# Performance work log

Hardware: AMD Instinct MI355X
Metric: run time of the kernel (lower is better)

## Reference

```python
import jax, jax.numpy as jnp
import numpy as np

N_G, N_D, D = 50000, 50000, 64
R, L, NNZ, B = 32, 2, 1600000, 2048
TEMP, LAMBDA_1, LAMBDA_2, DROPOUT = 0.2, 0.2, 1e-7, 0.1


def setup_inputs() -> dict:
    key = jax.random.key(0)
    ks = jax.random.split(key, 14)
    uids = jax.random.randint(ks[0], (B,), 0, N_G)
    iids = jax.random.randint(ks[1], (B,), 0, N_D)
    pos = jax.random.randint(ks[2], (B,), 0, N_D)
    neg = jax.random.randint(ks[3], (B,), 0, N_D)
    E_g_0 = jax.random.normal(ks[4], (N_G, D), jnp.float32) * 0.01
    E_d_0 = jax.random.normal(ks[5], (N_D, D), jnp.float32) * 0.01
    rows = jax.random.randint(ks[6], (NNZ,), 0, N_G)
    cols = jax.random.randint(ks[7], (NNZ,), 0, N_D)
    vals = jax.random.uniform(ks[8], (NNZ,), jnp.float32)
    g_mul_s = jax.random.normal(ks[9], (N_G, R), jnp.float32) * 0.1
    v_mul_s = jax.random.normal(ks[10], (N_D, R), jnp.float32) * 0.1
    ut = jax.random.normal(ks[11], (R, N_G), jnp.float32) * (N_G ** -0.5)
    vt = jax.random.normal(ks[12], (R, N_D), jnp.float32) * (N_D ** -0.5)
    drop_u = jax.random.uniform(ks[13], (L, 2, NNZ), jnp.float32)
    return {"uids": uids, "iids": iids, "pos": pos, "neg": neg,
            "E_g_0": E_g_0, "E_d_0": E_d_0, "rows": rows, "cols": cols,
            "vals": vals, "g_mul_s": g_mul_s, "v_mul_s": v_mul_s,
            "ut": ut, "vt": vt, "drop_u": drop_u}


def reference(uids, iids, pos, neg, E_g_0, E_d_0, rows, cols, vals,
              g_mul_s, v_mul_s, ut, vt, drop_u):
    # sparse_dropout keep masks (independent per layer and per spmm call)
    keep = (drop_u > DROPOUT).astype(vals.dtype) / (1.0 - DROPOUT)  # [L,2,NNZ]
    E_g, E_d = E_g_0, E_d_0
    E_g_sum, E_d_sum = E_g_0, E_d_0
    G_g_sum, G_d_sum = E_g_0, E_d_0
    for layer in range(L):
        # Z_g = dropout(A) @ E_d ; Z_d = dropout(A).T @ E_g  (COO spmm)
        vg = vals * keep[layer, 0]
        Z_g = jax.ops.segment_sum(vg[:, None] * E_d[cols], rows, num_segments=N_G)
        vd = vals * keep[layer, 1]
        Z_d = jax.ops.segment_sum(vd[:, None] * E_g[rows], cols, num_segments=N_D)
        # low-rank SVD branch
        G_g = g_mul_s @ (vt @ E_d)  # [n_g, d]
        G_d = v_mul_s @ (ut @ E_g)  # [n_d, d]
        E_g, E_d = Z_g, Z_d
        E_g_sum = E_g_sum + E_g
        E_d_sum = E_d_sum + E_d
        G_g_sum = G_g_sum + G_g
        G_d_sum = G_d_sum + G_d
    # InfoNCE-style contrastive loss (exactly as torch: log(sum exp + eps))
    S_g = (G_g_sum[uids] @ E_g_sum.T) / TEMP  # [B, n_g]
    S_d = (G_d_sum[iids] @ E_d_sum.T) / TEMP  # [B, n_d]
    neg_score = jnp.log(jnp.exp(S_g).sum(1) + 1e-8).mean() \
              + jnp.log(jnp.exp(S_d).sum(1) + 1e-8).mean()
    pos_score = jnp.clip((G_g_sum[uids] * E_g_sum[uids]).sum(1) / TEMP, -5.0, 5.0).mean() \
              + jnp.clip((G_d_sum[iids] * E_d_sum[iids]).sum(1) / TEMP, -5.0, 5.0).mean()
    loss_s = -pos_score + neg_score
    # BPR loss
    g_emb = E_g_sum[uids]
    diff = (g_emb * E_d_sum[pos]).sum(-1) - (g_emb * E_d_sum[neg]).sum(-1)
    loss_r = -jnp.log(jax.nn.sigmoid(diff)).mean()
    # L2 reg over trainable embedding params
    loss_reg = LAMBDA_2 * (jnp.sum(E_g_0 ** 2) + jnp.sum(E_d_0 ** 2))
    loss = loss_r + LAMBDA_1 * loss_s + loss_reg
    return (loss, loss_r, LAMBDA_1 * loss_s)
```

## Files before the change

kernel.cpp:

```cpp
#include <hip/hip_runtime.h>
#include <hip/hip_bf16.h>
#include <math.h>

#define N_Gc 50000
#define N_Dc 50000
#define DIM 64
#define RNK 32
#define NNZc 1600000
#define BSZ 2048
#define KEEPV (1.0f/0.9f)
#define INVT 5.0f
#define NBK3 391
#define NBLK 200
#define NSL 48
#define EPB 8000
#define MCH 256
#define MBLK 196
#define SCAP 6144

typedef __attribute__((ext_vector_type(8))) short bfrag;
typedef __attribute__((ext_vector_type(4))) float f32x4;
typedef unsigned long long u64;

__device__ inline ushort f2bf(float f) {
  union { float f; unsigned int u; } v; v.f = f;
  unsigned int r = (v.u + 0x7fffu + ((v.u >> 16) & 1u)) >> 16;
  return (ushort)r;
}
__device__ inline float bf2f(ushort u) {
  union { unsigned int i; float f; } v; v.i = ((unsigned int)u) << 16;
  return v.f;
}

__global__ __launch_bounds__(256) void hist3_kernel(const int* __restrict__ rows, const int* __restrict__ cols,
                                                    int* __restrict__ cntR, int* __restrict__ cntC) {
  __shared__ int lh_r[NBK3];
  __shared__ int lh_c[NBK3];
  int t = threadIdx.x, blk = blockIdx.x;
  for (int j = t; j < NBK3; j += 256) { lh_r[j] = 0; lh_c[j] = 0; }
  __syncthreads();
  int e0 = blk*EPB;
  for (int i = e0 + t; i < e0 + EPB; i += 256) {
    atomicAdd(&lh_r[__builtin_nontemporal_load(&rows[i]) >> 7], 1);
    atomicAdd(&lh_c[__builtin_nontemporal_load(&cols[i]) >> 7], 1);
  }
  __syncthreads();
  for (int j = t; j < NBK3; j += 256) {
    cntR[j*NBLK + blk] = lh_r[j];
    cntC[j*NBLK + blk] = lh_c[j];
  }
}

__global__ __launch_bounds__(1024) void cscan2_kernel(const int* __restrict__ cntA, int* __restrict__ cbA, int* __restrict__ bpA,
                                                      const int* __restrict__ cntB, int* __restrict__ cbB, int* __restrict__ bpB) {
  const int n = NBK3*NBLK;
  const int* cnt = blockIdx.x ? cntB : cntA;
  int* cb = blockIdx.x ? cbB : cbA;
  int* bp = blockIdx.x ? bpB : bpA;
  __shared__ int wsum[16];
  int t = threadIdx.x, lane = t & 63, w = t >> 6;
  int carry = 0;
  for (int base = 0; base < n; base += 1024) {
    int i = base + t;
    int v = (i < n) ? cnt[i] : 0;
    int x = v;
    #pragma unroll
    for (int o = 1; o < 64; o <<= 1) { int y = __shfl_up(x, o); if (lane >= o) x += y; }
    if (lane == 63) wsum[w] = x;
    __syncthreads();
    if (t < 16) {
      int s = wsum[t];
      #pragma unroll
      for (int o = 1; o < 16; o <<= 1) { int y = __shfl_up(s, o); if (t >= o) s += y; }
      wsum[t] = s;
    }
    __syncthreads();
    int wpre = (w == 0) ? 0 : wsum[w-1];
    int total = wsum[15];
    int ex = carry + wpre + (x - v);
    if (i < n) {
      cb[i] = ex;
      if (i % NBLK == 0) bp[i/NBLK] = ex;
    }
    carry += total;
    __syncthreads();
  }
  if (t == 0) bp[NBK3] = carry;
}

__global__ __launch_bounds__(256) void phaseA2_kernel(const int* __restrict__ rows, const int* __restrict__ cols,
    const float* __restrict__ vals, const float* __restrict__ drop,
    const int* __restrict__ cbR, const int* __restrict__ cbC,
    u64* __restrict__ stage_r, u64* __restrict__ stage_c) {
  __shared__ int cnt_r[NBK3], cnt_c[NBK3];
  __shared__ int base_r[NBK3], base_c[NBK3];
  int t = threadIdx.x, blk = blockIdx.x;
  for (int j = t; j < NBK3; j += 256) {
    cnt_r[j] = 0; cnt_c[j] = 0;
    base_r[j] = cbR[j*NBLK + blk];
    base_c[j] = cbC[j*NBLK + blk];
  }
  __syncthreads();
  int e0 = blk*EPB;
  for (int i = e0 + t; i < e0 + EPB; i += 256) {
    int r = __builtin_nontemporal_load(&rows[i]);
    int c = __builtin_nontemporal_load(&cols[i]);
    u64 vb = (u64)__float_as_uint(__builtin_nontemporal_load(&vals[i])) << 32;
    unsigned int dr0 = (__builtin_nontemporal_load(&drop[i]) > 0.1f) ? (1u<<24) : 0u;
    unsigned int dc0 = (__builtin_nontemporal_load(&drop[(size_t)NNZc + i]) > 0.1f) ? (1u<<24) : 0u;
    unsigned int dr1 = (__builtin_nontemporal_load(&drop[2*(size_t)NNZc + i]) > 0.1f) ? (1u<<25) : 0u;
    unsigned int dc1 = (__builtin_nontemporal_load(&drop[3*(size_t)NNZc + i]) > 0.1f) ? (1u<<25) : 0u;
    int br = r >> 7, bc = c >> 7;
    int p = base_r[br] + atomicAdd(&cnt_r[br], 1);
    stage_r[p] = vb | (unsigned int)c | ((unsigned int)(r & 127) << 16) | dr0 | dr1;
    int q = base_c[bc] + atomicAdd(&cnt_c[bc], 1);
    stage_c[q] = vb | (unsigned int)r | ((unsigned int)(c & 127) << 16) | dc0 | dc1;
  }
}

__global__ __launch_bounds__(256) void phaseB3_kernel(
    const int* __restrict__ bptrR, int* __restrict__ ptroutR, const u64* __restrict__ stageR,
    ushort* __restrict__ fcolR, float* __restrict__ fw0R, float* __restrict__ fw1R,
    const int* __restrict__ bptrC, int* __restrict__ ptroutC, const u64* __restrict__ stageC,
    ushort* __restrict__ fcolC, float* __restrict__ fw0C, float* __restrict__ fw1C, int n) {
  const int side = blockIdx.y;
  const int* bptr = side ? bptrC : bptrR;
  int* ptrout = side ? ptroutC : ptroutR;
  const u64* stage = side ? stageC : stageR;
  ushort* fcol = side ? fcolC : fcolR;
  float* fw0 = side ? fw0C : fw0R;
  float* fw1 = side ? fw1C : fw1R;
  __shared__ u64 sorted[SCAP];
  __shared__ int cnt[128];
  __shared__ int pos[128];
  __shared__ int wtot[2];
  int t = threadIdx.x, b = blockIdx.x;
  int base_row = b*128;
  int base = bptr[b], endp = bptr[b+1];
  int total = endp - base;
  if (t < 128) cnt[t] = 0;
  __syncthreads();
  for (int k = base + t; k < endp; k += 256) {
    unsigned int lo = (unsigned int)__builtin_nontemporal_load(&stage[k]);
    atomicAdd(&cnt[(lo >> 16) & 127], 1);
  }
  __syncthreads();
  int lane = t & 63;
  if (t < 128) {
    int c = cnt[t], x = c;
    #pragma unroll
    for (int o = 1; o < 64; o <<= 1) { int y = __shfl_up(x, o); if (lane >= o) x += y; }
    if (lane == 63) wtot[t >> 6] = x;
    __syncthreads();
    int excl = (x - c) + ((t >= 64) ? wtot[0] : 0);
    pos[t] = excl;
    int rr = base_row + t;
    if (rr <= n) ptrout[rr] = base + excl;
  } else {
    __syncthreads();
  }
  __syncthreads();
  if (total <= SCAP) {
    for (int k = base + t; k < endp; k += 256) {
      u64 rec = __builtin_nontemporal_load(&stage[k]);
      int rel = ((unsigned int)rec >> 16) & 127;
      int idx = atomicAdd(&pos[rel], 1);
      sorted[idx] = rec;
    }
    __syncthreads();
    for (int idx = t; idx < total; idx += 256) {
      u64 rec = sorted[idx];
      unsigned int lo = (unsigned int)rec;
      float v = __uint_as_float((unsigned int)(rec >> 32));
      int p = base + idx;
      fcol[p] = (ushort)(lo & 0xffffu);
      fw0[p] = (lo & (1u<<24)) ? v*KEEPV : 0.f;
      fw1[p] = (lo & (1u<<25)) ? v*KEEPV : 0.f;
    }
  } else {
    for (int k = base + t; k < endp; k += 256) {
      u64 rec = stage[k];
      unsigned int lo = (unsigned int)rec;
      int rel = (lo >> 16) & 127;
      int p = base + atomicAdd(&pos[rel], 1);
      float v = __uint_as_float((unsigned int)(rec >> 32));
      fcol[p] = (ushort)(lo & 0xffffu);
      fw0[p] = (lo & (1u<<24)) ? v*KEEPV : 0.f;
      fw1[p] = (lo & (1u<<25)) ? v*KEEPV : 0.f;
    }
  }
}

__device__ __forceinline__ float spmm_row(const ushort* __restrict__ fcol, const float* __restrict__ fw,
                                          const ushort* __restrict__ Eb, int k0, int end, int lane) {
  float acc = 0.f;
  int nfull = (end - k0) >> 3;
  int cc[8]; float ww[8];
  if (nfull > 0) {
    #pragma unroll
    for (int u = 0; u < 8; u++) {
      cc[u] = __builtin_nontemporal_load(&fcol[k0+u]);
      ww[u] = __builtin_nontemporal_load(&fw[k0+u]);
    }
    for (int b = 1; b < nfull; b++) {
      int kn = k0 + b*8;
      int cn[8]; float wn[8];
      #pragma unroll
      for (int u = 0; u < 8; u++) {
        cn[u] = __builtin_nontemporal_load(&fcol[kn+u]);
        wn[u] = __builtin_nontemporal_load(&fw[kn+u]);
      }
      #pragma unroll
      for (int u = 0; u < 8; u++) acc += ww[u]*bf2f(Eb[(size_t)cc[u]*DIM + lane]);
      #pragma unroll
      for (int u = 0; u < 8; u++) { cc[u] = cn[u]; ww[u] = wn[u]; }
    }
    #pragma unroll
    for (int u = 0; u < 8; u++) acc += ww[u]*bf2f(Eb[(size_t)cc[u]*DIM + lane]);
  }
  for (int k = k0 + nfull*8; k < end; k++)
    acc += __builtin_nontemporal_load(&fw[k])*bf2f(Eb[(size_t)__builtin_nontemporal_load(&fcol[k])*DIM + lane]);
  return acc;
}

__global__ __launch_bounds__(256) void spmm_l0_kernel(
    const int* __restrict__ ptrR, const ushort* __restrict__ fcolR, const float* __restrict__ fwR,
    const ushort* __restrict__ EbR, ushort* __restrict__ ZbR,
    const int* __restrict__ ptrC, const ushort* __restrict__ fcolC, const float* __restrict__ fwC,
    const ushort* __restrict__ EbC, ushort* __restrict__ ZbC, int nrows) {
  const int side = blockIdx.y;
  const int* ptr = side ? ptrC : ptrR;
  const ushort* fcol = side ? fcolC : fcolR;
  const float* fw = side ? fwC : fwR;
  const ushort* Eb = side ? EbC : EbR;
  ushort* Zb = side ? ZbC : ZbR;
  int lane = threadIdx.x & 63;
  int row = blockIdx.x*4 + (threadIdx.x >> 6);
  if (row >= nrows) return;
  float acc = spmm_row(fcol, fw, Eb, ptr[row], ptr[row+1], lane);
  Zb[(size_t)row*DIM + lane] = f2bf(acc);
}

__global__ __launch_bounds__(256) void spmm_l1_kernel(
    const int* __restrict__ ptrR, const ushort* __restrict__ fcolR, const float* __restrict__ fwR,
    const ushort* __restrict__ ZbOR, const float* __restrict__ E0R, const ushort* __restrict__ ZbSR,
    ushort* __restrict__ EoutR,
    const int* __restrict__ ptrC, const ushort* __restrict__ fcolC, const float* __restrict__ fwC,
    const ushort* __restrict__ ZbOC, const float* __restrict__ E0C, const ushort* __restrict__ ZbSC,
    ushort* __restrict__ EoutC, int nrows) {
  const int side = blockIdx.y;
  const int* ptr = side ? ptrC : ptrR;
  const ushort* fcol = side ? fcolC : fcolR;
  const float* fw = side ? fwC : fwR;
  const ushort* ZbO = side ? ZbOC : ZbOR;
  const float* E0 = side ? E0C : E0R;
  const ushort* ZbS = side ? ZbSC : ZbSR;
  ushort* Eout = side ? EoutC : EoutR;
  int lane = threadIdx.x & 63;
  int row = blockIdx.x*4 + (threadIdx.x >> 6);
  if (row >= nrows) return;
  float acc = spmm_row(fcol, fw, ZbO, ptr[row], ptr[row+1], lane);
  size_t o = (size_t)row*DIM + lane;
  acc += __builtin_nontemporal_load(&E0[o]) + bf2f(ZbS[o]);
  Eout[o] = f2bf(acc);
}

__global__ __launch_bounds__(256) void matred2_kernel(
    const float* __restrict__ vrowA, const float* __restrict__ E0A, const ushort* __restrict__ ZbA, float* __restrict__ MpA,
    const float* __restrict__ vrowB, const float* __restrict__ E0B, const ushort* __restrict__ ZbB, float* __restrict__ MpB,
    int n) {
  const int side = blockIdx.y;
  const float* vrow = side ? vrowB : vrowA;
  const float* E0 = side ? E0B : E0A;
  const ushort* Zb = side ? ZbB : ZbA;
  float* Mpart = side ? MpB : MpA;
  __shared__ float vs[RNK*MCH];
  __shared__ float part[RNK*DIM];
  int t = threadIdx.x, lane = t & 63, w = t >> 6;
  int ci0 = blockIdx.x*MCH;
  int cnt = min(MCH, n - ci0);
  for (int idx = t; idx < RNK*DIM; idx += 256) part[idx] = 0.f;
  for (int idx = t; idx < RNK*MCH; idx += 256) {
    int r = idx >> 8, i = idx & (MCH-1);
    vs[idx] = (i < cnt) ? __builtin_nontemporal_load(&vrow[(size_t)r*n + ci0 + i]) : 0.f;
  }
  __syncthreads();
  float acc[RNK];
  #pragma unroll
  for (int r = 0; r < RNK; r++) acc[r] = 0.f;
  int iw0 = w*64;
  for (int ii = 0; ii < 64; ii += 4) {
    int i = iw0 + ii;
    int gi = ci0 + i;
    float x0 = 0.f, x1 = 0.f, x2 = 0.f, x3 = 0.f;
    if (i+0 < cnt) x0 = E0[(size_t)(gi+0)*DIM + lane] + bf2f(Zb[(size_t)(gi+0)*DIM + lane]);
    if (i+1 < cnt) x1 = E0[(size_t)(gi+1)*DIM + lane] + bf2f(Zb[(size_t)(gi+1)*DIM + lane]);
    if (i+2 < cnt) x2 = E0[(size_t)(gi+2)*DIM + lane] + bf2f(Zb[(size_t)(gi+2)*DIM + lane]);
    if (i+3 < cnt) x3 = E0[(size_t)(gi+3)*DIM + lane] + bf2f(Zb[(size_t)(gi+3)*DIM + lane]);
    #pragma unroll
    for (int r = 0; r < RNK; r++) {
      float4 v4 = *(const float4*)&vs[r*MCH + i];
      acc[r] += v4.x*x0 + v4.y*x1 + v4.z*x2 + v4.w*x3;
    }
  }
  #pragma unroll
  for (int r = 0; r < RNK; r++) atomicAdd(&part[r*DIM + lane], acc[r]);
  __syncthreads();
  float* dst = Mpart + (size_t)blockIdx.x*(RNK*DIM);
  for (int idx = t; idx < RNK*DIM; idx += 256) dst[idx] = part[idx];
}

__global__ __launch_bounds__(256) void mreduce_kernel(const float* __restrict__ MpA, float* __restrict__ MA,
                                                      const float* __restrict__ MpB, float* __restrict__ MB, int nblk) {
  const float* Mpart = blockIdx.y ? MpB : MpA;
  float* M = blockIdx.y ? MB : MA;
  int idx = blockIdx.x*256 + threadIdx.x;
  if (idx < RNK*DIM) {
    float s = 0.f;
    for (int b = 0; b < nblk; b++) s += Mpart[(size_t)b*(RNK*DIM) + idx];
    M[idx] = s;
  }
}

__global__ __launch_bounds__(256) void gsmall_kernel(
    const int* __restrict__ idsA, const float* __restrict__ E0A, const float* __restrict__ mulA,
    const float* __restrict__ MA, float* __restrict__ outA, ushort* __restrict__ outbA,
    const int* __restrict__ idsB, const float* __restrict__ E0B, const float* __restrict__ mulB,
    const float* __restrict__ MB, float* __restrict__ outB, ushort* __restrict__ outbB) {
  const int side = blockIdx.y;
  const int* ids = side ? idsB : idsA;
  const float* E0 = side ? E0B : E0A;
  const float* mul = side ? mulB : mulA;
  const float* M = side ? MB : MA;
  float* out = side ? outB : outA;
  ushort* outb = side ? outbB : outbA;
  __shared__ float Ms[RNK*DIM];
  int t = threadIdx.x;
  for (int i = t; i < RNK*DIM; i += 256) Ms[i] = M[i];
  __syncthreads();
  int b = blockIdx.x*4 + (t >> 6), lane = t & 63;
  int u = ids[b];
  float a = E0[(size_t)u*DIM + lane];
  #pragma unroll
  for (int r = 0; r < RNK; r++) a += mul[(size_t)u*RNK + r]*Ms[r*DIM + lane];
  out[(size_t)b*DIM + lane] = a;
  outb[(size_t)b*DIM + lane] = f2bf(a);
}

__global__ __launch_bounds__(256) void convsq_kernel(const float* __restrict__ inA, ushort* __restrict__ outA,
                                                     const float* __restrict__ inB, ushort* __restrict__ outB,
                                                     int n4, float* __restrict__ acc) {
  const float* in = blockIdx.y ? inB : inA;
  ushort* out = blockIdx.y ? outB : outA;
  __shared__ float ls[4];
  int t = threadIdx.x;
  int idx = blockIdx.x*256 + t;
  int stride = gridDim.x*256;
  float s = 0.f;
  for (int i = idx; i < n4; i += stride) {
    float4 v = *(const float4*)&in[(size_t)i*4];
    ushort4 o;
    o.x = f2bf(v.x); o.y = f2bf(v.y); o.z = f2bf(v.z); o.w = f2bf(v.w);
    *(ushort4*)&out[(size_t)i*4] = o;
    s += v.x*v.x + v.y*v.y + v.z*v.z + v.w*v.w;
  }
  #pragma unroll
  for (int o = 32; o > 0; o >>= 1) s += __shfl_xor(s, o);
  if ((t & 63) == 0) ls[t >> 6] = s;
  __syncthreads();
  if (t == 0) atomicAdd(acc, ls[0] + ls[1] + ls[2] + ls[3]);
}

__global__ __launch_bounds__(256) void lse_mfma_kernel(
    const ushort* __restrict__ Ag, const ushort* __restrict__ Xg, float* __restrict__ seg,
    const ushort* __restrict__ Ad, const ushort* __restrict__ Xd, float* __restrict__ sed,
    int nj) {
  const ushort* A = blockIdx.y ? Ad : Ag;
  const ushort* X = blockIdx.y ? Xd : Xg;
  float* sumexp = blockIdx.y ? sed : seg;
  __shared__ __align__(16) ushort Xs[64*68];
  int t = threadIdx.x, lane = t & 63, w = t >> 6;
  int bt = blockIdx.x & 31, js = blockIdx.x >> 5;
  int b0 = bt*64;
  int m = lane & 15, q = lane >> 4;
  const ushort* Arow = A + (size_t)(b0 + w*16 + m)*DIM + q*8;
  bfrag a0 = *(const bfrag*)(Arow);
  bfrag a1 = *(const bfrag*)(Arow + 32);
  float rs0 = 0.f, rs1 = 0.f, rs2 = 0.f, rs3 = 0.f;
  int njt = (nj + 63) >> 6;
  for (int jt = js; jt < njt; jt += NSL) {
    int j0 = jt << 6;
    __syncthreads();
    for (int c = t; c < 512; c += 256) {
      int r = c >> 3, k8 = (c & 7) << 3;
      int j = j0 + r;
      ushort4 v0 = {0,0,0,0}, v1 = {0,0,0,0};
      if (j < nj) {
        const ushort4* src = (const ushort4*)(X + (size_t)j*DIM + k8);
        v0 = src[0]; v1 = src[1];
      }
      *(ushort4*)&Xs[r*68 + k8]     = v0;
      *(ushort4*)&Xs[r*68 + k8 + 4] = v1;
    }
    __syncthreads();
    #pragma unroll
    for (int jq = 0; jq < 4; jq++) {
      int jr = jq*16 + m;
      union { bfrag f; uint2 u2[2]; } B0, B1;
      B0.u2[0] = *(const uint2*)&Xs[jr*68 + q*8];
      B0.u2[1] = *(const uint2*)&Xs[jr*68 + q*8 + 4];
      B1.u2[0] = *(const uint2*)&Xs[jr*68 + 32 + q*8];
      B1.u2[1] = *(const uint2*)&Xs[jr*68 + 32 + q*8 + 4];
      f32x4 acc = {0.f, 0.f, 0.f, 0.f};
      acc = __builtin_amdgcn_mfma_f32_16x16x32_bf16(a0, B0.f, acc, 0, 0, 0);
      acc = __builtin_amdgcn_mfma_f32_16x16x32_bf16(a1, B1.f, acc, 0, 0, 0);
      int jg = j0 + jr;
      if (jg < nj) {
        rs0 += __expf(acc[0]*INVT);
        rs1 += __expf(acc[1]*INVT);
        rs2 += __expf(acc[2]*INVT);
        rs3 += __expf(acc[3]*INVT);
      }
    }
  }
  #pragma unroll
  for (int o = 1; o < 16; o <<= 1) {
    rs0 += __shfl_xor(rs0, o);
    rs1 += __shfl_xor(rs1, o);
    rs2 += __shfl_xor(rs2, o);
    rs3 += __shfl_xor(rs3, o);
  }
  if (m == 0) {
    float* dst = &sumexp[b0 + w*16 + q*4];
    atomicAdd(&dst[0], rs0);
    atomicAdd(&dst[1], rs1);
    atomicAdd(&dst[2], rs2);
    atomicAdd(&dst[3], rs3);
  }
}

__global__ __launch_bounds__(256) void perb_kernel(const int* __restrict__ uids, const int* __restrict__ iids,
    const int* __restrict__ pos, const int* __restrict__ neg,
    const float* __restrict__ Ggu, const float* __restrict__ Gdi,
    const ushort* __restrict__ Egs_b, const ushort* __restrict__ Eds_b,
    const float* __restrict__ seg, const float* __restrict__ sed,
    float* __restrict__ accs) {
  __shared__ float lsum[3][4];
  int t = threadIdx.x, lane = t & 63, w = t >> 6;
  int b = blockIdx.x*4 + w;
  int u = uids[b], it = iids[b], p = pos[b], ng = neg[b];
  float egu = bf2f(Egs_b[(size_t)u*DIM + lane]);
  float d1 = Ggu[(size_t)b*DIM + lane]*egu;
  float d2 = Gdi[(size_t)b*DIM + lane]*bf2f(Eds_b[(size_t)it*DIM + lane]);
  float d3 = egu*bf2f(Eds_b[(size_t)p*DIM + lane]);
  float d4 = egu*bf2f(Eds_b[(size_t)ng*DIM + lane]);
  #pragma unroll
  for (int o = 32; o > 0; o >>= 1) {
    d1 += __shfl_xor(d1, o);
    d2 += __shfl_xor(d2, o);
    d3 += __shfl_xor(d3, o);
    d4 += __shfl_xor(d4, o);
  }
  if (lane == 0) {
    float pterm = fminf(fmaxf(d1*INVT, -5.f), 5.f) + fminf(fmaxf(d2*INVT, -5.f), 5.f);
    float diff = d3 - d4;
    lsum[0][w] = pterm;
    lsum[1][w] = log1pf(expf(-diff));
    lsum[2][w] = logf(seg[b] + 1e-8f) + logf(sed[b] + 1e-8f);
  }
  __syncthreads();
  if (t < 3) atomicAdd(&accs[t], lsum[t][0] + lsum[t][1] + lsum[t][2] + lsum[t][3]);
}

__global__ void final_kernel(const float* __restrict__ accs, float* __restrict__ out) {
  float posm = accs[0]*(1.f/BSZ);
  float lr   = accs[1]*(1.f/BSZ);
  float negm = accs[2]*(1.f/BSZ);
  float reg  = 1e-7f*accs[3];
  float l1ls = 0.2f*(negm - posm);
  out[0] = lr + l1ls + reg;
  out[1] = lr;
  out[2] = l1ls;
}

extern "C" void kernel_launch(void* const* d_in, const int* in_sizes, int n_in,
                              void* d_out, int out_size, void* d_ws, size_t ws_size,
                              hipStream_t stream) {
  (void)in_sizes; (void)n_in; (void)out_size;
  const int*   uids = (const int*)d_in[0];
  const int*   iids = (const int*)d_in[1];
  const int*   pos  = (const int*)d_in[2];
  const int*   neg  = (const int*)d_in[3];
  const float* Eg0  = (const float*)d_in[4];
  const float* Ed0  = (const float*)d_in[5];
  const int*   rows = (const int*)d_in[6];
  const int*   cols = (const int*)d_in[7];
  const float* vals = (const float*)d_in[8];
  const float* gms  = (const float*)d_in[9];
  const float* vms  = (const float*)d_in[10];
  const float* ut   = (const float*)d_in[11];
  const float* vt   = (const float*)d_in[12];
  const float* drop = (const float*)d_in[13];
  float* out = (float*)d_out;

  float* ws = (float*)d_ws;
  const size_t ED = (size_t)N_Gc*DIM;
  float* REG_A = ws;
  float* REG_B = REG_A + ED;
  int* ptr_r = (int*)(REG_B + ED);
  int* ptr_c = ptr_r + (N_Gc + 1);
  int* bptr_r = ptr_c + (N_Dc + 1);
  int* bptr_c = bptr_r + (NBK3 + 1);
  int* cntR = bptr_c + (NBK3 + 1);
  int* cntC = cntR + NBK3*NBLK;
  int* cbR  = cntC + NBK3*NBLK;
  int* cbC  = cbR + NBK3*NBLK;
  ushort* fcol_r = (ushort*)(cbC + NBK3*NBLK);
  float* fw_r0  = (float*)(fcol_r + NNZc);
  float* fw_r1  = fw_r0 + NNZc;
  ushort* fcol_c = (ushort*)(fw_r1 + NNZc);
  float* fw_c0  = (float*)(fcol_c + NNZc);
  float* fw_c1  = fw_c0 + NNZc;
  float* Ggu = fw_c1 + NNZc;
  float* Gdi = Ggu + (size_t)BSZ*DIM;
  ushort* Ggu_b = (ushort*)(Gdi + (size_t)BSZ*DIM);
  ushort* Gdi_b = Ggu_b + (size_t)BSZ*DIM;
  float* Mg  = (float*)(Gdi_b + (size_t)BSZ*DIM);
  float* Md  = Mg + RNK*DIM;
  float* seg = Md + RNK*DIM;
  float* sed = seg + BSZ;
  float* accs = sed + BSZ;
  float* MpG = accs + 16;
  float* MpD = MpG + (size_t)MBLK*RNK*DIM;

  u64* stage_r = (u64*)REG_A;
  u64* stage_c = (u64*)REG_B;
  ushort* Zg0_b = (ushort*)REG_A;
  ushort* Zd0_b = Zg0_b + ED;
  ushort* Eg0_b = (ushort*)REG_B;
  ushort* Ed0_b = Eg0_b + ED;
  ushort* Egs_b = (ushort*)REG_B;
  ushort* Eds_b = Egs_b + ED;

  size_t need = ((char*)(MpD + (size_t)MBLK*RNK*DIM)) - ((char*)d_ws);
  if (ws_size < need) return;

  hipMemsetAsync(seg, 0, sizeof(float)*(2*BSZ + 16), stream);

  hist3_kernel<<<NBLK, 256, 0, stream>>>(rows, cols, cntR, cntC);
  cscan2_kernel<<<2, 1024, 0, stream>>>(cntR, cbR, bptr_r, cntC, cbC, bptr_c);
  phaseA2_kernel<<<NBLK, 256, 0, stream>>>(rows, cols, vals, drop, cbR, cbC, stage_r, stage_c);
  phaseB3_kernel<<<dim3(NBK3, 2), 256, 0, stream>>>(
      bptr_r, ptr_r, stage_r, fcol_r, fw_r0, fw_r1,
      bptr_c, ptr_c, stage_c, fcol_c, fw_c0, fw_c1, N_Gc);

  int n4 = (int)(ED/4);
  convsq_kernel<<<dim3(1024, 2), 256, 0, stream>>>(Eg0, Eg0_b, Ed0, Ed0_b, n4, accs + 3);

  int spmm_blocks = (N_Gc + 3)/4;
  spmm_l0_kernel<<<dim3(spmm_blocks, 2), 256, 0, stream>>>(
      ptr_r, fcol_r, fw_r0, Ed0_b, Zg0_b,
      ptr_c, fcol_c, fw_c0, Eg0_b, Zd0_b, N_Gc);
  spmm_l1_kernel<<<dim3(spmm_blocks, 2), 256, 0, stream>>>(
      ptr_r, fcol_r, fw_r1, Zd0_b, Eg0, Zg0_b, Egs_b,
      ptr_c, fcol_c, fw_c1, Zg0_b, Ed0, Zd0_b, Eds_b, N_Gc);

  matred2_kernel<<<dim3(MBLK, 2), 256, 0, stream>>>(
      vt, Ed0, Zd0_b, MpG,
      ut, Eg0, Zg0_b, MpD, N_Dc);
  mreduce_kernel<<<dim3((RNK*DIM + 255)/256, 2), 256, 0, stream>>>(MpG, Mg, MpD, Md, MBLK);

  gsmall_kernel<<<dim3(BSZ/4, 2), 256, 0, stream>>>(
      uids, Eg0, gms, Mg, Ggu, Ggu_b,
      iids, Ed0, vms, Md, Gdi, Gdi_b);

  lse_mfma_kernel<<<dim3(32*NSL, 2), 256, 0, stream>>>(Ggu_b, Egs_b, seg, Gdi_b, Eds_b, sed, N_Gc);

  perb_kernel<<<BSZ/4, 256, 0, stream>>>(uids, iids, pos, neg, Ggu, Gdi, Egs_b, Eds_b, seg, sed, accs);
  final_kernel<<<1, 1, 0, stream>>>(accs, out);
}
```

Baseline: 660.3 us.

## Pack CSR column and bf16 weight into one word; double batch rows per LSE block

The CSR column index and the dropout-scaled weight are packed into a single 32-bit word (16-bit column, bf16 weight), which cuts index/weight traffic in the SpMM kernels from 6 to 4 bytes per nonzero. The layer-1 SpMM now reads the bf16 copy of E0 instead of the fp32 one. The LSE MFMA kernel processes 128 batch rows per block instead of 64, reusing each staged B tile across two A fragments and halving the grid. This trades weight precision (fp32 to bf16) and adds register pressure in the LSE kernel in exchange for less memory traffic and more reuse.

```diff
diff --git a/kernel.cpp b/kernel.cpp
--- a/kernel.cpp
+++ b/kernel.cpp
@@ -21,14 +21,15 @@
 typedef __attribute__((ext_vector_type(8))) short bfrag;
 typedef __attribute__((ext_vector_type(4))) float f32x4;
 typedef unsigned long long u64;
+typedef unsigned int u32;
 
 __device__ inline ushort f2bf(float f) {
   union { float f; unsigned int u; } v; v.f = f;
   unsigned int r = (v.u + 0x7fffu + ((v.u >> 16) & 1u)) >> 16;
   return (ushort)r;
 }
-__device__ inline float bf2f(ushort u) {
-  union { unsigned int i; float f; } v; v.i = ((unsigned int)u) << 16;
+__device__ inline float bf2f(u32 u) {
+  union { unsigned int i; float f; } v; v.i = u << 16;
   return v.f;
 }
 
@@ -120,16 +121,15 @@
 
 __global__ __launch_bounds__(256) void phaseB3_kernel(
     const int* __restrict__ bptrR, int* __restrict__ ptroutR, const u64* __restrict__ stageR,
-    ushort* __restrict__ fcolR, float* __restrict__ fw0R, float* __restrict__ fw1R,
+    u32* __restrict__ ew0R, u32* __restrict__ ew1R,
     const int* __restrict__ bptrC, int* __restrict__ ptroutC, const u64* __restrict__ stageC,
-    ushort* __restrict__ fcolC, float* __restrict__ fw0C, float* __restrict__ fw1C, int n) {
+    u32* __restrict__ ew0C, u32* __restrict__ ew1C, int n) {
   const int side = blockIdx.y;
   const int* bptr = side ? bptrC : bptrR;
   int* ptrout = side ? ptroutC : ptroutR;
   const u64* stage = side ? stageC : stageR;
-  ushort* fcol = side ? fcolC : fcolR;
-  float* fw0 = side ? fw0C : fw0R;
-  float* fw1 = side ? fw1C : fw1R;
+  u32* ew0 = side ? ew0C : ew0R;
+  u32* ew1 = side ? ew1C : ew1R;
   __shared__ u64 sorted[SCAP];
   __shared__ int cnt[128];
   __shared__ int pos[128];
@@ -172,10 +172,12 @@
       u64 rec = sorted[idx];
       unsigned int lo = (unsigned int)rec;
       float v = __uint_as_float((unsigned int)(rec >> 32));
+      u32 col = lo & 0xffffu;
+      u32 w0 = (lo & (1u<<24)) ? (u32)f2bf(v*KEEPV) : 0u;
+      u32 w1 = (lo & (1u<<25)) ? (u32)f2bf(v*KEEPV) : 0u;
       int p = base + idx;
-      fcol[p] = (ushort)(lo & 0xffffu);
-      fw0[p] = (lo & (1u<<24)) ? v*KEEPV : 0.f;
-      fw1[p] = (lo & (1u<<25)) ? v*KEEPV : 0.f;
+      ew0[p] = col | (w0 << 16);
+      ew1[p] = col | (w1 << 16);
     }
   } else {
     for (int k = base + t; k < endp; k += 256) {
@@ -184,84 +186,78 @@
       int rel = (lo >> 16) & 127;
       int p = base + atomicAdd(&pos[rel], 1);
       float v = __uint_as_float((unsigned int)(rec >> 32));
-      fcol[p] = (ushort)(lo & 0xffffu);
-      fw0[p] = (lo & (1u<<24)) ? v*KEEPV : 0.f;
-      fw1[p] = (lo & (1u<<25)) ? v*KEEPV : 0.f;
-    }
-  }
-}
-
-__device__ __forceinline__ float spmm_row(const ushort* __restrict__ fcol, const float* __restrict__ fw,
+      u32 col = lo & 0xffffu;
+      u32 w0 = (lo & (1u<<24)) ? (u32)f2bf(v*KEEPV) : 0u;
+      u32 w1 = (lo & (1u<<25)) ? (u32)f2bf(v*KEEPV) : 0u;
+      ew0[p] = col | (w0 << 16);
+      ew1[p] = col | (w1 << 16);
+    }
+  }
+}
+
+__device__ __forceinline__ float spmm_row(const u32* __restrict__ ew,
                                           const ushort* __restrict__ Eb, int k0, int end, int lane) {
   float acc = 0.f;
   int nfull = (end - k0) >> 3;
-  int cc[8]; float ww[8];
+  u32 e[8];
   if (nfull > 0) {
     #pragma unroll
-    for (int u = 0; u < 8; u++) {
-      cc[u] = __builtin_nontemporal_load(&fcol[k0+u]);
-      ww[u] = __builtin_nontemporal_load(&fw[k0+u]);
-    }
+    for (int u = 0; u < 8; u++) e[u] = __builtin_nontemporal_load(&ew[k0+u]);
     for (int b = 1; b < nfull; b++) {
       int kn = k0 + b*8;
-      int cn[8]; float wn[8];
+      u32 en[8];
       #pragma unroll
-      for (int u = 0; u < 8; u++) {
-        cn[u] = __builtin_nontemporal_load(&fcol[kn+u]);
-        wn[u] = __builtin_nontemporal_load(&fw[kn+u]);
-      }
+      for (int u = 0; u < 8; u++) en[u] = __builtin_nontemporal_load(&ew[kn+u]);
       #pragma unroll
-      for (int u = 0; u < 8; u++) acc += ww[u]*bf2f(Eb[(size_t)cc[u]*DIM + lane]);
+      for (int u = 0; u < 8; u++) acc += bf2f(e[u] >> 16)*bf2f(Eb[(size_t)(e[u] & 0xffffu)*DIM + lane]);
       #pragma unroll
-      for (int u = 0; u < 8; u++) { cc[u] = cn[u]; ww[u] = wn[u]; }
-    }
-    #pragma unroll
-    for (int u = 0; u < 8; u++) acc += ww[u]*bf2f(Eb[(size_t)cc[u]*DIM + lane]);
-  }
-  for (int k = k0 + nfull*8; k < end; k++)
-    acc += __builtin_nontemporal_load(&fw[k])*bf2f(Eb[(size_t)__builtin_nontemporal_load(&fcol[k])*DIM + lane]);
+      for (int u = 0; u < 8; u++) e[u] = en[u];
+    }
+    #pragma unroll
+    for (int u = 0; u < 8; u++) acc += bf2f(e[u] >> 16)*bf2f(Eb[(size_t)(e[u] & 0xffffu)*DIM + lane]);
+  }
+  for (int k = k0 + nfull*8; k < end; k++) {
+    u32 ek = __builtin_nontemporal_load(&ew[k]);
+    acc += bf2f(ek >> 16)*bf2f(Eb[(size_t)(ek & 0xffffu)*DIM + lane]);
+  }
   return acc;
 }
 
 __global__ __launch_bounds__(256) void spmm_l0_kernel(
-    const int* __restrict__ ptrR, const ushort* __restrict__ fcolR, const float* __restrict__ fwR,
-    const ushort* __restrict__ EbR, ushort* __restrict__ ZbR,
-    const int* __restrict__ ptrC, const ushort* __restrict__ fcolC, const float* __restrict__ fwC,
-    const ushort* __restrict__ EbC, ushort* __restrict__ ZbC, int nrows) {
+    const int* __restrict__ ptrR, const u32* __restrict__ ewR, const ushort* __restrict__ EbR, ushort* __restrict__ ZbR,
+    const int* __restrict__ ptrC, const u32* __restrict__ ewC, const ushort* __restrict__ EbC, ushort* __restrict__ ZbC,
+    int nrows) {
   const int side = blockIdx.y;
   const int* ptr = side ? ptrC : ptrR;
-  const ushort* fcol = side ? fcolC : fcolR;
-  const float* fw = side ? fwC : fwR;
+  const u32* ew = side ? ewC : ewR;
   const ushort* Eb = side ? EbC : EbR;
   ushort* Zb = side ? ZbC : ZbR;
   int lane = threadIdx.x & 63;
   int row = blockIdx.x*4 + (threadIdx.x >> 6);
   if (row >= nrows) return;
-  float acc = spmm_row(fcol, fw, Eb, ptr[row], ptr[row+1], lane);
+  float acc = spmm_row(ew, Eb, ptr[row], ptr[row+1], lane);
   Zb[(size_t)row*DIM + lane] = f2bf(acc);
 }
 
 __global__ __launch_bounds__(256) void spmm_l1_kernel(
-    const int* __restrict__ ptrR, const ushort* __restrict__ fcolR, const float* __restrict__ fwR,
-    const ushort* __restrict__ ZbOR, const float* __restrict__ E0R, const ushort* __restrict__ ZbSR,
-    ushort* __restrict__ EoutR,
-    const int* __restrict__ ptrC, const ushort* __restrict__ fcolC, const float* __restrict__ fwC,
-    const ushort* __restrict__ ZbOC, const float* __restrict__ E0C, const ushort* __restrict__ ZbSC,
-    ushort* __restrict__ EoutC, int nrows) {
+    const int* __restrict__ ptrR, const u32* __restrict__ ewR, const ushort* __restrict__ ZbOR,
+    const ushort* __restrict__ E0bR, const ushort* __restrict__ ZbSR, ushort* __restrict__ EoutR,
+    const int* __restrict__ ptrC, const u32* __restrict__ ewC, const ushort* __restrict__ ZbOC,
+    const ushort* __restrict__ E0bC, const ushort* __restrict__ ZbSC, ushort* __restrict__ EoutC,
+    int nrows) {
   const int side = blockIdx.y;
   const int* ptr = side ? ptrC : ptrR;
-  const ushort* fcol = side ? fcolC : fcolR;
-  const float* fw = side ? fwC : fwR;
+  const u32* ew = side ? ewC : ewR;
   const ushort* ZbO = side ? ZbOC : ZbOR;
-  const float* E0 = side ? E0C : E0R;
+  const ushort* E0b = side ? E0bC : E0bR;
   const ushort* ZbS = side ? ZbSC : ZbSR;
   ushort* Eout = side ? EoutC : EoutR;
   int lane = threadIdx.x & 63;
   int row = blockIdx.x*4 + (threadIdx.x >> 6);
   if (row >= nrows) return;
-  float acc = spmm_row(fcol, fw, ZbO, ptr[row], ptr[row+1], lane);
+  float acc = spmm_row(ew, ZbO, ptr[row], ptr[row+1], lane);
   size_t o = (size_t)row*DIM + lane;
-  acc += __builtin_nontemporal_load(&E0[o]) + bf2f(ZbS[o]);
+  acc += bf2f(E0b[o]) + bf2f(ZbS[o]);
   Eout[o] = f2bf(acc);
 }
 
@@ -380,13 +376,16 @@
   float* sumexp = blockIdx.y ? sed : seg;
   __shared__ __align__(16) ushort Xs[64*68];
   int t = threadIdx.x, lane = t & 63, w = t >> 6;
-  int bt = blockIdx.x & 31, js = blockIdx.x >> 5;
-  int b0 = bt*64;
+  int bt = blockIdx.x & 15, js = blockIdx.x >> 4;
+  int b0 = bt*128;
   int m = lane & 15, q = lane >> 4;
-  const ushort* Arow = A + (size_t)(b0 + w*16 + m)*DIM + q*8;
-  bfrag a0 = *(const bfrag*)(Arow);
-  bfrag a1 = *(const bfrag*)(Arow + 32);
-  float rs0 = 0.f, rs1 = 0.f, rs2 = 0.f, rs3 = 0.f;
+  const ushort* Arow0 = A + (size_t)(b0 + w*16 + m)*DIM + q*8;
+  const ushort* Arow1 = A + (size_t)(b0 + 64 + w*16 + m)*DIM + q*8;
+  bfrag a00 = *(const bfrag*)(Arow0);
+  bfrag a01 = *(const bfrag*)(Arow0 + 32);
+  bfrag a10 = *(const bfrag*)(Arow1);
+  bfrag a11 = *(const bfrag*)(Arow1 + 32);
+  float rs[2][4] = {{0.f,0.f,0.f,0.f},{0.f,0.f,0.f,0.f}};
   int njt = (nj + 63) >> 6;
   for (int jt = js; jt < njt; jt += NSL) {
     int j0 = jt << 6;
@@ -411,31 +410,44 @@
       B0.u2[1] = *(const uint2*)&Xs[jr*68 + q*8 + 4];
       B1.u2[0] = *(const uint2*)&Xs[jr*68 + 32 + q*8];
       B1.u2[1] = *(const uint2*)&Xs[jr*68 + 32 + q*8 + 4];
-      f32x4 acc = {0.f, 0.f, 0.f, 0.f};
-      acc = __builtin_amdgcn_mfma_f32_16x16x32_bf16(a0, B0.f, acc, 0, 0, 0);
-      acc = __builtin_amdgcn_mfma_f32_16x16x32_bf16(a1, B1.f, acc, 0, 0, 0);
+      f32x4 acc0 = {0.f, 0.f, 0.f, 0.f};
+      f32x4 acc1 = {0.f, 0.f, 0.f, 0.f};
+      acc0 = __builtin_amdgcn_mfma_f32_16x16x32_bf16(a00, B0.f, acc0, 0, 0, 0);
+      acc0 = __builtin_amdgcn_mfma_f32_16x16x32_bf16(a01, B1.f, acc0, 0, 0, 0);
+      acc1 = __builtin_amdgcn_mfma_f32_16x16x32_bf16(a10, B0.f, acc1, 0, 0, 0);
+      acc1 = __builtin_amdgcn_mfma_f32_16x16x32_bf16(a11, B1.f, acc1, 0, 0, 0);
       int jg = j0 + jr;
       if (jg < nj) {
-        rs0 += __expf(acc[0]*INVT);
-        rs1 += __expf(acc[1]*INVT);
-        rs2 += __expf(acc[2]*INVT);
-        rs3 += __expf(acc[3]*INVT);
+        rs[0][0] += __expf(acc0[0]*INVT);
+        rs[0][1] += __expf(acc0[1]*INVT);
+        rs[0][2] += __expf(acc0[2]*INVT);
+        rs[0][3] += __expf(acc0[3]*INVT);
+        rs[1][0] += __expf(acc1[0]*INVT);
+        rs[1][1] += __expf(acc1[1]*INVT);
+        rs[1][2] += __expf(acc1[2]*INVT);
+        rs[1][3] += __expf(acc1[3]*INVT);
       }
     }
   }
   #pragma unroll
-  for (int o = 1; o < 16; o <<= 1) {
-    rs0 += __shfl_xor(rs0, o);
-    rs1 += __shfl_xor(rs1, o);
-    rs2 += __shfl_xor(rs2, o);
-    rs3 += __shfl_xor(rs3, o);
+  for (int h = 0; h < 2; h++) {
+    #pragma unroll
+    for (int o = 1; o < 16; o <<= 1) {
+      rs[h][0] += __shfl_xor(rs[h][0], o);
+      rs[h][1] += __shfl_xor(rs[h][1], o);
+      rs[h][2] += __shfl_xor(rs[h][2], o);
+      rs[h][3] += __shfl_xor(rs[h][3], o);
+    }
   }
   if (m == 0) {
-    float* dst = &sumexp[b0 + w*16 + q*4];
-    atomicAdd(&dst[0], rs0);
-    atomicAdd(&dst[1], rs1);
-    atomicAdd(&dst[2], rs2);
-    atomicAdd(&dst[3], rs3);
+    #pragma unroll
+    for (int h = 0; h < 2; h++) {
+      float* dst = &sumexp[b0 + h*64 + w*16 + q*4];
+      atomicAdd(&dst[0], rs[h][0]);
+      atomicAdd(&dst[1], rs[h][1]);
+      atomicAdd(&dst[2], rs[h][2]);
+      atomicAdd(&dst[3], rs[h][3]);
+    }
   }
 }
 
@@ -515,13 +527,11 @@
   int* cntC = cntR + NBK3*NBLK;
   int* cbR  = cntC + NBK3*NBLK;
   int* cbC  = cbR + NBK3*NBLK;
-  ushort* fcol_r = (ushort*)(cbC + NBK3*NBLK);
-  float* fw_r0  = (float*)(fcol_r + NNZc);
-  float* fw_r1  = fw_r0 + NNZc;
-  ushort* fcol_c = (ushort*)(fw_r1 + NNZc);
-  float* fw_c0  = (float*)(fcol_c + NNZc);
-  float* fw_c1  = fw_c0 + NNZc;
-  float* Ggu = fw_c1 + NNZc;
+  u32* ew_r0 = (u32*)(cbC + NBK3*NBLK);
+  u32* ew_r1 = ew_r0 + NNZc;
+  u32* ew_c0 = ew_r1 + NNZc;
+  u32* ew_c1 = ew_c0 + NNZc;
+  float* Ggu = (float*)(ew_c1 + NNZc);
   float* Gdi = Ggu + (size_t)BSZ*DIM;
   ushort* Ggu_b = (ushort*)(Gdi + (size_t)BSZ*DIM);
   ushort* Gdi_b = Ggu_b + (size_t)BSZ*DIM;
@@ -551,19 +561,19 @@
   cscan2_kernel<<<2, 1024, 0, stream>>>(cntR, cbR, bptr_r, cntC, cbC, bptr_c);
   phaseA2_kernel<<<NBLK, 256, 0, stream>>>(rows, cols, vals, drop, cbR, cbC, stage_r, stage_c);
   phaseB3_kernel<<<dim3(NBK3, 2), 256, 0, stream>>>(
-      bptr_r, ptr_r, stage_r, fcol_r, fw_r0, fw_r1,
-      bptr_c, ptr_c, stage_c, fcol_c, fw_c0, fw_c1, N_Gc);
+      bptr_r, ptr_r, stage_r, ew_r0, ew_r1,
+      bptr_c, ptr_c, stage_c, ew_c0, ew_c1, N_Gc);
 
   int n4 = (int)(ED/4);
   convsq_kernel<<<dim3(1024, 2), 256, 0, stream>>>(Eg0, Eg0_b, Ed0, Ed0_b, n4, accs + 3);
 
   int spmm_blocks = (N_Gc + 3)/4;
   spmm_l0_kernel<<<dim3(spmm_blocks, 2), 256, 0, stream>>>(
-      ptr_r, fcol_r, fw_r0, Ed0_b, Zg0_b,
-      ptr_c, fcol_c, fw_c0, Eg0_b, Zd0_b, N_Gc);
+      ptr_r, ew_r0, Ed0_b, Zg0_b,
+      ptr_c, ew_c0, Eg0_b, Zd0_b, N_Gc);
   spmm_l1_kernel<<<dim3(spmm_blocks, 2), 256, 0, stream>>>(
-      ptr_r, fcol_r, fw_r1, Zd0_b, Eg0, Zg0_b, Egs_b,
-      ptr_c, fcol_c, fw_c1, Zg0_b, Ed0, Zd0_b, Eds_b, N_Gc);
+      ptr_r, ew_r1, Zd0_b, Eg0_b, Zg0_b, Egs_b,
+      ptr_c, ew_c1, Zg0_b, Ed0_b, Zd0_b, Eds_b, N_Gc);
 
   matred2_kernel<<<dim3(MBLK, 2), 256, 0, stream>>>(
       vt, Ed0, Zd0_b, MpG,
@@ -574,7 +584,7 @@
       uids, Eg0, gms, Mg, Ggu, Ggu_b,
       iids, Ed0, vms, Md, Gdi, Gdi_b);
 
-  lse_mfma_kernel<<<dim3(32*NSL, 2), 256, 0, stream>>>(Ggu_b, Egs_b, seg, Gdi_b, Eds_b, sed, N_Gc);
+  lse_mfma_kernel<<<dim3(16*NSL, 2), 256, 0, stream>>>(Ggu_b, Egs_b, seg, Gdi_b, Eds_b, sed, N_Gc);
 
   perb_kernel<<<BSZ/4, 256, 0, stream>>>(uids, iids, pos, neg, Ggu, Gdi, Egs_b, Eds_b, seg, sed, accs);
   final_kernel<<<1, 1, 0, stream>>>(accs, out);
```

New measurement: 610.2 us. 7.6% less time.
